# Kernel tuning notes

Measured on AMD Instinct MI355X. Metric: run time of the kernel, lower is better.

Reference implementation:

```python
import jax, jax.numpy as jnp
import numpy as np

B, S, D_MODEL, D_K, D_V = 4, 2048, 1024, 1024, 1024


def setup_inputs() -> dict:
    key = jax.random.key(0)
    k1, k2, k3, k4 = jax.random.split(key, 4)
    scale = 1.0 / np.sqrt(D_MODEL)
    x = jax.random.normal(k1, (B, S, D_MODEL), dtype=jnp.float32)
    Wq = jax.random.normal(k2, (D_K, D_MODEL), dtype=jnp.float32) * scale
    Wk = jax.random.normal(k3, (D_K, D_MODEL), dtype=jnp.float32) * scale
    Wv = jax.random.normal(k4, (D_V, D_MODEL), dtype=jnp.float32) * scale
    # causal mask: position i may attend to j <= i (True = keep)
    mask = jnp.broadcast_to(jnp.tril(jnp.ones((S, S), dtype=bool)), (B, S, S))
    return {"x": x, "mask": mask, "Wq": Wq, "Wk": Wk, "Wv": Wv}


def reference(x, mask, Wq, Wk, Wv):
    # nn.Linear(d, k, bias=False): y = x @ W.T with W of shape [k, d]
    q = jnp.einsum('bsd,kd->bsk', x, Wq)
    k = jnp.einsum('bsd,kd->bsk', x, Wk)
    v = jnp.einsum('bsd,vd->bsv', x, Wv)
    scores = jnp.einsum('bik,bjk->bij', q, k) / jnp.sqrt(jnp.float32(D_K))
    s = jnp.where(mask, scores, -jnp.inf)
    # masked, fully-masked-row-safe softmax (fully masked rows -> all zeros,
    # matching softmax[all-masked rows] = 0 in the original)
    m = jnp.max(s, axis=-1, keepdims=True)
    m_safe = jnp.where(jnp.isfinite(m), m, 0.0)
    e = jnp.exp(s - m_safe)          # exp(-inf) = 0 for masked entries
    denom = jnp.sum(e, axis=-1, keepdims=True)
    p = e / jnp.where(denom == 0.0, 1.0, denom)
    return jnp.einsum('bij,bjv->biv', p, v)
```

## Files before the change

### kernel.cpp

```cpp
#include <hip/hip_runtime.h>
#include <hip/hip_bf16.h>
#include <stdint.h>

#define SEQ   2048
#define DM    1024
#define NBAT  4

typedef __attribute__((ext_vector_type(8))) short  short8;
typedef __attribute__((ext_vector_type(4))) float  floatx4;

__device__ __forceinline__ unsigned short f2b(float f) {
    __hip_bfloat16 h = __float2bfloat16(f);
    unsigned short r;
    __builtin_memcpy(&r, &h, 2);
    return r;
}

__device__ __forceinline__ ushort4 pack4(float a, float b, float c, float d) {
    ushort4 u; u.x = f2b(a); u.y = f2b(b); u.z = f2b(c); u.w = f2b(d); return u;
}

__device__ __forceinline__ void gload16(const void* g, void* s) {
    __builtin_amdgcn_global_load_lds(
        (const __attribute__((address_space(1))) unsigned int*)(uintptr_t)g,
        (__attribute__((address_space(3))) unsigned int*)(uintptr_t)s,
        16, 0, 0);
}

__global__ void prep(const float4* __restrict__ x,
                     const float4* __restrict__ w0, const float4* __restrict__ w1,
                     const float4* __restrict__ w2,
                     ushort4* __restrict__ xb, ushort4* __restrict__ wall,
                     float* __restrict__ rsum)
{
    const int b = blockIdx.x;
    const int t = threadIdx.x;
    if (b < 8192) {
        const int i = b * 256 + t;
        float4 f = x[i];
        xb[i] = pack4(f.x, f.y, f.z, f.w);
    } else if (b < 11264) {
        const int idx  = b - 8192;
        const int wsel = idx >> 10;
        const int i    = (idx & 1023) * 256 + t;
        const float4* src = (wsel == 0) ? w0 : (wsel == 1) ? w1 : w2;
        float4 f = src[i];
        wall[(size_t)wsel * 262144 + i] = pack4(f.x, f.y, f.z, f.w);
    } else {
        rsum[(b - 11264) * 256 + t] = 0.f;
    }
}

#define SLOTS 24576

__global__ __launch_bounds__(512, 2) void qkv_gemm(
    const unsigned short* __restrict__ A, const unsigned short* __restrict__ Bm,
    unsigned short* __restrict__ Qo, unsigned short* __restrict__ Ko,
    unsigned short* __restrict__ Vto, float qscale)
{
    __shared__ __align__(16) unsigned short lds[3 * SLOTS];

    const int bid = blockIdx.x;
    const int wg  = (bid & 7) * 96 + (bid >> 3);
    const int mt  = wg / 24, nt = wg - mt * 24;
    const int m0  = mt * 256, n0 = nt * 128;

    const int t    = threadIdx.x;
    const int w    = t >> 6;
    const int lane = t & 63;
    const int wr   = w >> 1, wc = w & 1;
    const int r    = lane & 15, q = lane >> 4;

    const int srow = lane >> 3;
    const int scol = ((lane & 7) ^ srow) << 3;

    const int aoff = (wr >> 1) * 8192 + ((wr & 1) * 64 + r) * 64;
    const int boff = 16384 + (wc * 64 + r) * 64;
    const int sk0  = ((0 + q) ^ (r & 7)) * 8;
    const int sk1  = ((4 + q) ^ (r & 7)) * 8;

    floatx4 acc[4][4];
#pragma unroll
    for (int i = 0; i < 4; i++)
#pragma unroll
        for (int j = 0; j < 4; j++)
            acc[i][j] = (floatx4){0.f, 0.f, 0.f, 0.f};

#define STGA(KB, SL) do { \
    gload16(A + (((size_t)(m0 +       w * 16 + srow)) << 10) + (KB) + scol, &lds[(SL) +         w * 1024]); \
    gload16(A + (((size_t)(m0 +   8 + w * 16 + srow)) << 10) + (KB) + scol, &lds[(SL) +         w * 1024 + 512]); \
    gload16(A + (((size_t)(m0 + 128 + w * 16 + srow)) << 10) + (KB) + scol, &lds[(SL) + 8192 +  w * 1024]); \
    gload16(A + (((size_t)(m0 + 136 + w * 16 + srow)) << 10) + (KB) + scol, &lds[(SL) + 8192 +  w * 1024 + 512]); \
  } while (0)
#define STGB(KB, SL) do { \
    gload16(Bm + (((size_t)(n0 +      w * 16 + srow)) << 10) + (KB) + scol, &lds[(SL) + 16384 + w * 1024]); \
    gload16(Bm + (((size_t)(n0 +  8 + w * 16 + srow)) << 10) + (KB) + scol, &lds[(SL) + 16384 + w * 1024 + 512]); \
  } while (0)

    STGA(0, 0);
    STGB(0, 0);
    STGA(64, SLOTS);
    STGB(64, SLOTS);
    asm volatile("s_waitcnt vmcnt(6)" ::: "memory");
    __builtin_amdgcn_s_barrier();

    for (int tt = 0; tt < 16; ++tt) {
        const int sl  = (tt % 3) * SLOTS;
        const int nsl = ((tt + 2) % 3) * SLOTS;
        const int nkb = (tt + 2 < 16) ? (tt + 2) * 64 : 0;

        const int aB = sl + aoff;
        const int bB = sl + boff;
        short8 a00 = *(const short8*)&lds[aB + sk0 +    0];
        short8 a10 = *(const short8*)&lds[aB + sk0 + 1024];
        short8 a20 = *(const short8*)&lds[aB + sk0 + 2048];
        short8 a30 = *(const short8*)&lds[aB + sk0 + 3072];
        short8 b00 = *(const short8*)&lds[bB + sk0 +    0];
        short8 b10 = *(const short8*)&lds[bB + sk0 + 1024];
        short8 b20 = *(const short8*)&lds[bB + sk0 + 2048];
        short8 b30 = *(const short8*)&lds[bB + sk0 + 3072];
        short8 a01 = *(const short8*)&lds[aB + sk1 +    0];
        short8 a11 = *(const short8*)&lds[aB + sk1 + 1024];
        short8 a21 = *(const short8*)&lds[aB + sk1 + 2048];
        short8 a31 = *(const short8*)&lds[aB + sk1 + 3072];
        short8 b01 = *(const short8*)&lds[bB + sk1 +    0];
        short8 b11 = *(const short8*)&lds[bB + sk1 + 1024];
        short8 b21 = *(const short8*)&lds[bB + sk1 + 2048];
        short8 b31 = *(const short8*)&lds[bB + sk1 + 3072];

        STGA(nkb, nsl);
        STGB(nkb, nsl);
        asm volatile("s_waitcnt vmcnt(6)" ::: "memory");
        __builtin_amdgcn_s_barrier();

        __builtin_amdgcn_s_setprio(1);
        acc[0][0] = __builtin_amdgcn_mfma_f32_16x16x32_bf16(a00, b00, acc[0][0], 0, 0, 0);
        acc[0][1] = __builtin_amdgcn_mfma_f32_16x16x32_bf16(a00, b10, acc[0][1], 0, 0, 0);
        acc[0][2] = __builtin_amdgcn_mfma_f32_16x16x32_bf16(a00, b20, acc[0][2], 0, 0, 0);
        acc[0][3] = __builtin_amdgcn_mfma_f32_16x16x32_bf16(a00, b30, acc[0][3], 0, 0, 0);
        acc[1][0] = __builtin_amdgcn_mfma_f32_16x16x32_bf16(a10, b00, acc[1][0], 0, 0, 0);
        acc[1][1] = __builtin_amdgcn_mfma_f32_16x16x32_bf16(a10, b10, acc[1][1], 0, 0, 0);
        acc[1][2] = __builtin_amdgcn_mfma_f32_16x16x32_bf16(a10, b20, acc[1][2], 0, 0, 0);
        acc[1][3] = __builtin_amdgcn_mfma_f32_16x16x32_bf16(a10, b30, acc[1][3], 0, 0, 0);
        acc[2][0] = __builtin_amdgcn_mfma_f32_16x16x32_bf16(a20, b00, acc[2][0], 0, 0, 0);
        acc[2][1] = __builtin_amdgcn_mfma_f32_16x16x32_bf16(a20, b10, acc[2][1], 0, 0, 0);
        acc[2][2] = __builtin_amdgcn_mfma_f32_16x16x32_bf16(a20, b20, acc[2][2], 0, 0, 0);
        acc[2][3] = __builtin_amdgcn_mfma_f32_16x16x32_bf16(a20, b30, acc[2][3], 0, 0, 0);
        acc[3][0] = __builtin_amdgcn_mfma_f32_16x16x32_bf16(a30, b00, acc[3][0], 0, 0, 0);
        acc[3][1] = __builtin_amdgcn_mfma_f32_16x16x32_bf16(a30, b10, acc[3][1], 0, 0, 0);
        acc[3][2] = __builtin_amdgcn_mfma_f32_16x16x32_bf16(a30, b20, acc[3][2], 0, 0, 0);
        acc[3][3] = __builtin_amdgcn_mfma_f32_16x16x32_bf16(a30, b30, acc[3][3], 0, 0, 0);
        acc[0][0] = __builtin_amdgcn_mfma_f32_16x16x32_bf16(a01, b01, acc[0][0], 0, 0, 0);
        acc[0][1] = __builtin_amdgcn_mfma_f32_16x16x32_bf16(a01, b11, acc[0][1], 0, 0, 0);
        acc[0][2] = __builtin_amdgcn_mfma_f32_16x16x32_bf16(a01, b21, acc[0][2], 0, 0, 0);
        acc[0][3] = __builtin_amdgcn_mfma_f32_16x16x32_bf16(a01, b31, acc[0][3], 0, 0, 0);
        acc[1][0] = __builtin_amdgcn_mfma_f32_16x16x32_bf16(a11, b01, acc[1][0], 0, 0, 0);
        acc[1][1] = __builtin_amdgcn_mfma_f32_16x16x32_bf16(a11, b11, acc[1][1], 0, 0, 0);
        acc[1][2] = __builtin_amdgcn_mfma_f32_16x16x32_bf16(a11, b21, acc[1][2], 0, 0, 0);
        acc[1][3] = __builtin_amdgcn_mfma_f32_16x16x32_bf16(a11, b31, acc[1][3], 0, 0, 0);
        acc[2][0] = __builtin_amdgcn_mfma_f32_16x16x32_bf16(a21, b01, acc[2][0], 0, 0, 0);
        acc[2][1] = __builtin_amdgcn_mfma_f32_16x16x32_bf16(a21, b11, acc[2][1], 0, 0, 0);
        acc[2][2] = __builtin_amdgcn_mfma_f32_16x16x32_bf16(a21, b21, acc[2][2], 0, 0, 0);
        acc[2][3] = __builtin_amdgcn_mfma_f32_16x16x32_bf16(a21, b31, acc[2][3], 0, 0, 0);
        acc[3][0] = __builtin_amdgcn_mfma_f32_16x16x32_bf16(a31, b01, acc[3][0], 0, 0, 0);
        acc[3][1] = __builtin_amdgcn_mfma_f32_16x16x32_bf16(a31, b11, acc[3][1], 0, 0, 0);
        acc[3][2] = __builtin_amdgcn_mfma_f32_16x16x32_bf16(a31, b21, acc[3][2], 0, 0, 0);
        acc[3][3] = __builtin_amdgcn_mfma_f32_16x16x32_bf16(a31, b31, acc[3][3], 0, 0, 0);
        __builtin_amdgcn_s_setprio(0);
    }
#undef STGA
#undef STGB

    const int gmb = m0 + wr * 64 + q * 4;
    const int gnb = n0 + wc * 64 + r;
    if (nt < 8) {
#pragma unroll
        for (int i = 0; i < 4; i++) {
            const int gm = gmb + i * 16;
#pragma unroll
            for (int j = 0; j < 4; j++) {
                const int gn = gnb + j * 16;
#pragma unroll
                for (int rr = 0; rr < 4; rr++)
                    Qo[(size_t)(gm + rr) * 1024 + gn] = f2b(acc[i][j][rr] * qscale);
            }
        }
    } else if (nt < 16) {
#pragma unroll
        for (int i = 0; i < 4; i++) {
            const int gm = gmb + i * 16;
#pragma unroll
            for (int j = 0; j < 4; j++) {
                const int gn = gnb + j * 16;
#pragma unroll
                for (int rr = 0; rr < 4; rr++)
                    Ko[(size_t)(gm + rr) * 1024 + (gn - 1024)] = f2b(acc[i][j][rr]);
            }
        }
    } else {
#pragma unroll
        for (int i = 0; i < 4; i++) {
            const int gm = gmb + i * 16;
            const int b  = gm >> 11;
            const int s  = gm & 2047;
#pragma unroll
            for (int j = 0; j < 4; j++) {
                const int v = gnb + j * 16 - 2048;
                *(ushort4*)&Vto[((size_t)(b * 1024 + v)) * 2048 + s] =
                    pack4(acc[i][j][0], acc[i][j][1], acc[i][j][2], acc[i][j][3]);
            }
        }
    }
}

template<int MODE>
__global__ __launch_bounds__(512, 2) void attn256(
    const unsigned short* __restrict__ Ag, const unsigned short* __restrict__ Bg,
    void* __restrict__ Cv, float* __restrict__ rowsum)
{
    __shared__ __align__(16) unsigned short lds[3 * SLOTS];

    const int z = blockIdx.z;
    int m0, n0;
    if (MODE == 0) {
        const int f = blockIdx.x;
        int ti = (int)((sqrtf(4.f * f + 1.f) - 1.f) * 0.5f);
        while ((ti + 1) * (ti + 2) <= f) ti++;
        while (ti * (ti + 1) > f) ti--;
        const int tj = f - ti * (ti + 1);
        m0 = ti * 256;
        n0 = tj * 128;
    } else {
        m0 = (int)(gridDim.y - 1 - blockIdx.y) * 256;
        n0 = blockIdx.x * 128;
    }

    const size_t LDA = (MODE == 0) ? DM : SEQ;
    const size_t LDB = (MODE == 0) ? DM : SEQ;
    const unsigned short* A  = Ag + (size_t)z * ((MODE == 0) ? SEQ * DM : SEQ * SEQ);
    const unsigned short* Bm = Bg + (size_t)z * ((MODE == 0) ? SEQ * DM : DM * SEQ);
    const int NT = ((MODE == 0) ? DM : (m0 + 256)) / 64;

    const int t    = threadIdx.x;
    const int w    = t >> 6;
    const int lane = t & 63;
    const int wr   = w >> 1, wc = w & 1;
    const int r    = lane & 15, q = lane >> 4;

    const int srow = lane >> 3;
    const int scol = ((lane & 7) ^ srow) << 3;

    const int aoff = (wr >> 1) * 8192 + ((wr & 1) * 64 + r) * 64;
    const int boff = 16384 + (wc * 64 + r) * 64;
    const int sk0  = ((0 + q) ^ (r & 7)) * 8;
    const int sk1  = ((4 + q) ^ (r & 7)) * 8;

    floatx4 acc[4][4];
#pragma unroll
    for (int i = 0; i < 4; i++)
#pragma unroll
        for (int j = 0; j < 4; j++)
            acc[i][j] = (floatx4){0.f, 0.f, 0.f, 0.f};

#define ASTG(KB, SL) do { \
    gload16(A + (size_t)(m0 +       w * 16 + srow) * LDA + (KB) + scol, &lds[(SL) +         w * 1024]); \
    gload16(A + (size_t)(m0 +   8 + w * 16 + srow) * LDA + (KB) + scol, &lds[(SL) +         w * 1024 + 512]); \
    gload16(A + (size_t)(m0 + 128 + w * 16 + srow) * LDA + (KB) + scol, &lds[(SL) + 8192 +  w * 1024]); \
    gload16(A + (size_t)(m0 + 136 + w * 16 + srow) * LDA + (KB) + scol, &lds[(SL) + 8192 +  w * 1024 + 512]); \
  } while (0)
#define BSTG(KB, SL) do { \
    gload16(Bm + (size_t)(n0 +      w * 16 + srow) * LDB + (KB) + scol, &lds[(SL) + 16384 + w * 1024]); \
    gload16(Bm + (size_t)(n0 +  8 + w * 16 + srow) * LDB + (KB) + scol, &lds[(SL) + 16384 + w * 1024 + 512]); \
  } while (0)

    ASTG(0, 0);
    BSTG(0, 0);
    ASTG(64, SLOTS);
    BSTG(64, SLOTS);
    asm volatile("s_waitcnt vmcnt(6)" ::: "memory");
    __builtin_amdgcn_s_barrier();

    for (int tt = 0; tt < NT; ++tt) {
        const int sl  = (tt % 3) * SLOTS;
        const int nsl = ((tt + 2) % 3) * SLOTS;
        const int nkb = (tt + 2 < NT) ? (tt + 2) * 64 : 0;

        const int aB = sl + aoff;
        const int bB = sl + boff;
        short8 a00 = *(const short8*)&lds[aB + sk0 +    0];
        short8 a10 = *(const short8*)&lds[aB + sk0 + 1024];
        short8 a20 = *(const short8*)&lds[aB + sk0 + 2048];
        short8 a30 = *(const short8*)&lds[aB + sk0 + 3072];
        short8 b00 = *(const short8*)&lds[bB + sk0 +    0];
        short8 b10 = *(const short8*)&lds[bB + sk0 + 1024];
        short8 b20 = *(const short8*)&lds[bB + sk0 + 2048];
        short8 b30 = *(const short8*)&lds[bB + sk0 + 3072];
        short8 a01 = *(const short8*)&lds[aB + sk1 +    0];
        short8 a11 = *(const short8*)&lds[aB + sk1 + 1024];
        short8 a21 = *(const short8*)&lds[aB + sk1 + 2048];
        short8 a31 = *(const short8*)&lds[aB + sk1 + 3072];
        short8 b01 = *(const short8*)&lds[bB + sk1 +    0];
        short8 b11 = *(const short8*)&lds[bB + sk1 + 1024];
        short8 b21 = *(const short8*)&lds[bB + sk1 + 2048];
        short8 b31 = *(const short8*)&lds[bB + sk1 + 3072];

        ASTG(nkb, nsl);
        BSTG(nkb, nsl);
        asm volatile("s_waitcnt vmcnt(6)" ::: "memory");
        __builtin_amdgcn_s_barrier();

        __builtin_amdgcn_s_setprio(1);
        acc[0][0] = __builtin_amdgcn_mfma_f32_16x16x32_bf16(b00, a00, acc[0][0], 0, 0, 0);
        acc[0][1] = __builtin_amdgcn_mfma_f32_16x16x32_bf16(b10, a00, acc[0][1], 0, 0, 0);
        acc[0][2] = __builtin_amdgcn_mfma_f32_16x16x32_bf16(b20, a00, acc[0][2], 0, 0, 0);
        acc[0][3] = __builtin_amdgcn_mfma_f32_16x16x32_bf16(b30, a00, acc[0][3], 0, 0, 0);
        acc[1][0] = __builtin_amdgcn_mfma_f32_16x16x32_bf16(b00, a10, acc[1][0], 0, 0, 0);
        acc[1][1] = __builtin_amdgcn_mfma_f32_16x16x32_bf16(b10, a10, acc[1][1], 0, 0, 0);
        acc[1][2] = __builtin_amdgcn_mfma_f32_16x16x32_bf16(b20, a10, acc[1][2], 0, 0, 0);
        acc[1][3] = __builtin_amdgcn_mfma_f32_16x16x32_bf16(b30, a10, acc[1][3], 0, 0, 0);
        acc[2][0] = __builtin_amdgcn_mfma_f32_16x16x32_bf16(b00, a20, acc[2][0], 0, 0, 0);
        acc[2][1] = __builtin_amdgcn_mfma_f32_16x16x32_bf16(b10, a20, acc[2][1], 0, 0, 0);
        acc[2][2] = __builtin_amdgcn_mfma_f32_16x16x32_bf16(b20, a20, acc[2][2], 0, 0, 0);
        acc[2][3] = __builtin_amdgcn_mfma_f32_16x16x32_bf16(b30, a20, acc[2][3], 0, 0, 0);
        acc[3][0] = __builtin_amdgcn_mfma_f32_16x16x32_bf16(b00, a30, acc[3][0], 0, 0, 0);
        acc[3][1] = __builtin_amdgcn_mfma_f32_16x16x32_bf16(b10, a30, acc[3][1], 0, 0, 0);
        acc[3][2] = __builtin_amdgcn_mfma_f32_16x16x32_bf16(b20, a30, acc[3][2], 0, 0, 0);
        acc[3][3] = __builtin_amdgcn_mfma_f32_16x16x32_bf16(b30, a30, acc[3][3], 0, 0, 0);
        acc[0][0] = __builtin_amdgcn_mfma_f32_16x16x32_bf16(b01, a01, acc[0][0], 0, 0, 0);
        acc[0][1] = __builtin_amdgcn_mfma_f32_16x16x32_bf16(b11, a01, acc[0][1], 0, 0, 0);
        acc[0][2] = __builtin_amdgcn_mfma_f32_16x16x32_bf16(b21, a01, acc[0][2], 0, 0, 0);
        acc[0][3] = __builtin_amdgcn_mfma_f32_16x16x32_bf16(b31, a01, acc[0][3], 0, 0, 0);
        acc[1][0] = __builtin_amdgcn_mfma_f32_16x16x32_bf16(b01, a11, acc[1][0], 0, 0, 0);
        acc[1][1] = __builtin_amdgcn_mfma_f32_16x16x32_bf16(b11, a11, acc[1][1], 0, 0, 0);
        acc[1][2] = __builtin_amdgcn_mfma_f32_16x16x32_bf16(b21, a11, acc[1][2], 0, 0, 0);
        acc[1][3] = __builtin_amdgcn_mfma_f32_16x16x32_bf16(b31, a11, acc[1][3], 0, 0, 0);
        acc[2][0] = __builtin_amdgcn_mfma_f32_16x16x32_bf16(b01, a21, acc[2][0], 0, 0, 0);
        acc[2][1] = __builtin_amdgcn_mfma_f32_16x16x32_bf16(b11, a21, acc[2][1], 0, 0, 0);
        acc[2][2] = __builtin_amdgcn_mfma_f32_16x16x32_bf16(b21, a21, acc[2][2], 0, 0, 0);
        acc[2][3] = __builtin_amdgcn_mfma_f32_16x16x32_bf16(b31, a21, acc[2][3], 0, 0, 0);
        acc[3][0] = __builtin_amdgcn_mfma_f32_16x16x32_bf16(b01, a31, acc[3][0], 0, 0, 0);
        acc[3][1] = __builtin_amdgcn_mfma_f32_16x16x32_bf16(b11, a31, acc[3][1], 0, 0, 0);
        acc[3][2] = __builtin_amdgcn_mfma_f32_16x16x32_bf16(b21, a31, acc[3][2], 0, 0, 0);
        acc[3][3] = __builtin_amdgcn_mfma_f32_16x16x32_bf16(b31, a31, acc[3][3], 0, 0, 0);
        __builtin_amdgcn_s_setprio(0);
    }
#undef ASTG
#undef BSTG

    const int gmb = m0 + wr * 64 + r;
    const int gnb = n0 + wc * 64 + q * 4;
    if (MODE == 0) {
        unsigned short* E = (unsigned short*)Cv + (size_t)z * SEQ * SEQ;
        float* rs = rowsum + (size_t)z * SEQ;
#pragma unroll
        for (int i = 0; i < 4; i++) {
            const int gm = gmb + i * 16;
            float part = 0.f;
#pragma unroll
            for (int j = 0; j < 4; j++) {
                const int gn = gnb + j * 16;
                float e0 = (gn + 0 <= gm) ? __expf(acc[i][j][0]) : 0.f;
                float e1 = (gn + 1 <= gm) ? __expf(acc[i][j][1]) : 0.f;
                float e2 = (gn + 2 <= gm) ? __expf(acc[i][j][2]) : 0.f;
                float e3 = (gn + 3 <= gm) ? __expf(acc[i][j][3]) : 0.f;
                part += (e0 + e1) + (e2 + e3);
                *(ushort4*)&E[(size_t)gm * SEQ + gn] = pack4(e0, e1, e2, e3);
            }
            part += __shfl_xor(part, 16, 64);
            part += __shfl_xor(part, 32, 64);
            if (q == 0) atomicAdd(&rs[gm], part);
        }
    } else {
        float* C = (float*)Cv + (size_t)z * SEQ * DM;
        const float* rs = rowsum + (size_t)z * SEQ;
#pragma unroll
        for (int i = 0; i < 4; i++) {
            const int gm = gmb + i * 16;
            const float inv = 1.0f / rs[gm];
#pragma unroll
            for (int j = 0; j < 4; j++) {
                const int gn = gnb + j * 16;
                float4 o;
                o.x = acc[i][j][0] * inv;
                o.y = acc[i][j][1] * inv;
                o.z = acc[i][j][2] * inv;
                o.w = acc[i][j][3] * inv;
                *(float4*)&C[(size_t)gm * DM + gn] = o;
            }
        }
    }
}

extern "C" void kernel_launch(void* const* d_in, const int* in_sizes, int n_in,
                              void* d_out, int out_size, void* d_ws, size_t ws_size,
                              hipStream_t stream) {
    (void)in_sizes; (void)n_in; (void)out_size; (void)ws_size;
    const float* x  = (const float*)d_in[0];
    const float* Wq = (const float*)d_in[2];
    const float* Wk = (const float*)d_in[3];
    const float* Wv = (const float*)d_in[4];

    char* base = (char*)d_ws;
    size_t off = 0;
    auto alloc = [&](size_t n) { char* p = base + off; off += (n + 255) & ~(size_t)255; return p; };

    unsigned short* xb   = (unsigned short*)alloc((size_t)NBAT * SEQ * DM * 2);
    unsigned short* wall = (unsigned short*)alloc((size_t)3 * DM * DM * 2);
    unsigned short* Qb   = (unsigned short*)alloc((size_t)NBAT * SEQ * DM * 2);
    unsigned short* Kb   = (unsigned short*)alloc((size_t)NBAT * SEQ * DM * 2);
    unsigned short* Vtb  = (unsigned short*)alloc((size_t)NBAT * DM * SEQ * 2);
    unsigned short* E    = (unsigned short*)alloc((size_t)NBAT * SEQ * SEQ * 2);
    float*          rsum = (float*)alloc((size_t)NBAT * SEQ * 4);

    prep<<<dim3(11296), dim3(256), 0, stream>>>(
        (const float4*)x, (const float4*)Wq, (const float4*)Wk, (const float4*)Wv,
        (ushort4*)xb, (ushort4*)wall, rsum);

    qkv_gemm<<<dim3(768), dim3(512), 0, stream>>>(
        xb, wall, Qb, Kb, Vtb, 0.03125f);

    attn256<0><<<dim3(72, 1, NBAT), dim3(512), 0, stream>>>(Qb, Kb, E, rsum);

    attn256<1><<<dim3(DM / 128, SEQ / 256, NBAT), dim3(512), 0, stream>>>(E, Vtb, d_out, rsum);
}
```

Measured before the change: 260.5 us.

## Use 256x256 tiles with double buffering for QKV and QK^T GEMMs

Adds a new gemm256 kernel with 256x256 output tiles (8 waves, each holding an 8x4 MFMA accumulator grid) and a two-stage LDS double buffer. It replaces the 256x128 triple-buffered QKV projection and QK^T score kernels, halving their block counts. The larger tile raises arithmetic intensity and data reuse per load, at the cost of more accumulator registers and LDS per block. The causal QK^T kernel now runs on a triangular grid of 256x256 tiles. The PV kernel is kept with its original tiling.

```diff
diff --git a/kernel.cpp b/kernel.cpp
--- a/kernel.cpp
+++ b/kernel.cpp
@@ -51,19 +51,202 @@
     }
 }
 
+template<int EPI>
+__global__ __launch_bounds__(512, 2) void gemm256(
+    const unsigned short* __restrict__ Ag, const unsigned short* __restrict__ Bg,
+    void* __restrict__ P0, void* __restrict__ P1, void* __restrict__ P2,
+    float* __restrict__ rowsum, float qscale)
+{
+    __shared__ __align__(16) unsigned short lds[65536];
+
+    int m0, n0, ntl = 0, z = 0;
+    const unsigned short* A;
+    const unsigned short* Bm;
+
+    if (EPI == 0) {
+        const int bid = blockIdx.x;
+        const int wg  = (bid & 7) * 48 + (bid >> 3);
+        const int mt  = wg / 12; ntl = wg - mt * 12;
+        m0 = mt * 256; n0 = ntl * 256;
+        A = Ag; Bm = Bg;
+    } else {
+        z = blockIdx.z;
+        const int f = blockIdx.x;
+        int ti = (int)((sqrtf(8.f * f + 1.f) - 1.f) * 0.5f);
+        while ((ti + 1) * (ti + 2) / 2 <= f) ti++;
+        while (ti * (ti + 1) / 2 > f) ti--;
+        const int tj = f - ti * (ti + 1) / 2;
+        m0 = ti * 256; n0 = tj * 256;
+        A = Ag + (size_t)z * SEQ * DM; Bm = Bg + (size_t)z * SEQ * DM;
+    }
+
+    const int t    = threadIdx.x;
+    const int w    = t >> 6;
+    const int lane = t & 63;
+    const int wr   = w >> 2, wc = w & 3;
+    const int r    = lane & 15, q = lane >> 4;
+
+    const int srow = lane >> 3;
+    const int scol = ((lane & 7) ^ srow) << 3;
+
+    const int sk0 = ((0 + q) ^ (r & 7)) * 8;
+    const int sk1 = ((4 + q) ^ (r & 7)) * 8;
+    const int aRd = wr * 8192 + r * 64;
+    const int bRd = 16384 + (wc >> 1) * 8192 + ((wc & 1) * 64 + r) * 64;
+
+    floatx4 acc[8][4];
+#pragma unroll
+    for (int i = 0; i < 8; i++)
+#pragma unroll
+        for (int j = 0; j < 4; j++)
+            acc[i][j] = (floatx4){0.f, 0.f, 0.f, 0.f};
+
+#define STGC(G, R0, KB, CB) do { \
+    gload16((G) + (size_t)((R0) + w * 16 + srow)     * DM + (KB) + scol, &lds[(CB) + w * 1024]); \
+    gload16((G) + (size_t)((R0) + w * 16 + srow + 8) * DM + (KB) + scol, &lds[(CB) + w * 1024 + 512]); \
+  } while (0)
+#define STG4(KB, OB) do { \
+    STGC(A,  m0,       (KB), (OB)); \
+    STGC(A,  m0 + 128, (KB), (OB) + 8192); \
+    STGC(Bm, n0,       (KB), (OB) + 16384); \
+    STGC(Bm, n0 + 128, (KB), (OB) + 24576); \
+  } while (0)
+
+#define ONE_MFMA(AC, AF, BF) do { \
+    if (EPI == 0) (AC) = __builtin_amdgcn_mfma_f32_16x16x32_bf16((AF), (BF), (AC), 0, 0, 0); \
+    else          (AC) = __builtin_amdgcn_mfma_f32_16x16x32_bf16((BF), (AF), (AC), 0, 0, 0); \
+  } while (0)
+
+    STG4(0, 0);
+
+    for (int tt = 0; tt < 16; ++tt) {
+        const int cb  = (tt & 1) * 32768;
+        const int ob  = 32768 - cb;
+        const int nkb = (tt + 1 < 16 ? tt + 1 : 0) * 64;
+
+        asm volatile("s_waitcnt vmcnt(0)" ::: "memory");
+        __builtin_amdgcn_s_barrier();
+
+        short8 a0[8], b0[4];
+#pragma unroll
+        for (int i = 0; i < 8; i++)
+            a0[i] = *(const short8*)&lds[cb + aRd + i * 1024 + sk0];
+#pragma unroll
+        for (int j = 0; j < 4; j++)
+            b0[j] = *(const short8*)&lds[cb + bRd + j * 1024 + sk0];
+
+        STG4(nkb, ob);
+
+        __builtin_amdgcn_s_setprio(1);
+#pragma unroll
+        for (int i = 0; i < 8; i++)
+#pragma unroll
+            for (int j = 0; j < 4; j++)
+                ONE_MFMA(acc[i][j], a0[i], b0[j]);
+
+        short8 a1[8], b1[4];
+#pragma unroll
+        for (int i = 0; i < 8; i++)
+            a1[i] = *(const short8*)&lds[cb + aRd + i * 1024 + sk1];
+#pragma unroll
+        for (int j = 0; j < 4; j++)
+            b1[j] = *(const short8*)&lds[cb + bRd + j * 1024 + sk1];
+#pragma unroll
+        for (int i = 0; i < 8; i++)
+#pragma unroll
+            for (int j = 0; j < 4; j++)
+                ONE_MFMA(acc[i][j], a1[i], b1[j]);
+        __builtin_amdgcn_s_setprio(0);
+    }
+#undef STGC
+#undef STG4
+#undef ONE_MFMA
+
+    if (EPI == 0) {
+        const int gmb = m0 + wr * 128 + q * 4;
+        const int gnb = n0 + wc * 64 + r;
+        unsigned short* Qo  = (unsigned short*)P0;
+        unsigned short* Ko  = (unsigned short*)P1;
+        unsigned short* Vto = (unsigned short*)P2;
+        if (ntl < 4) {
+#pragma unroll
+            for (int i = 0; i < 8; i++) {
+                const int gm = gmb + i * 16;
+#pragma unroll
+                for (int j = 0; j < 4; j++) {
+                    const int gn = gnb + j * 16;
+#pragma unroll
+                    for (int rr = 0; rr < 4; rr++)
+                        Qo[(size_t)(gm + rr) * 1024 + gn] = f2b(acc[i][j][rr] * qscale);
+                }
+            }
+        } else if (ntl < 8) {
+#pragma unroll
+            for (int i = 0; i < 8; i++) {
+                const int gm = gmb + i * 16;
+#pragma unroll
+                for (int j = 0; j < 4; j++) {
+                    const int gn = gnb + j * 16;
+#pragma unroll
+                    for (int rr = 0; rr < 4; rr++)
+                        Ko[(size_t)(gm + rr) * 1024 + (gn - 1024)] = f2b(acc[i][j][rr]);
+                }
+            }
+        } else {
+#pragma unroll
+            for (int i = 0; i < 8; i++) {
+                const int gm = gmb + i * 16;
+                const int b  = gm >> 11;
+                const int s  = gm & 2047;
+#pragma unroll
+                for (int j = 0; j < 4; j++) {
+                    const int v = gnb + j * 16 - 2048;
+                    *(ushort4*)&Vto[((size_t)(b * 1024 + v)) * 2048 + s] =
+                        pack4(acc[i][j][0], acc[i][j][1], acc[i][j][2], acc[i][j][3]);
+                }
+            }
+        }
+    } else {
+        const int gmb = m0 + wr * 128 + r;
+        const int gnb = n0 + wc * 64 + q * 4;
+        unsigned short* E = (unsigned short*)P0 + (size_t)z * SEQ * SEQ;
+        float* rs = rowsum + (size_t)z * SEQ;
+#pragma unroll
+        for (int i = 0; i < 8; i++) {
+            const int gm = gmb + i * 16;
+            float part = 0.f;
+#pragma unroll
+            for (int j = 0; j < 4; j++) {
+                const int gn = gnb + j * 16;
+                float e0 = (gn + 0 <= gm) ? __expf(acc[i][j][0]) : 0.f;
+                float e1 = (gn + 1 <= gm) ? __expf(acc[i][j][1]) : 0.f;
+                float e2 = (gn + 2 <= gm) ? __expf(acc[i][j][2]) : 0.f;
+                float e3 = (gn + 3 <= gm) ? __expf(acc[i][j][3]) : 0.f;
+                part += (e0 + e1) + (e2 + e3);
+                *(ushort4*)&E[(size_t)gm * SEQ + gn] = pack4(e0, e1, e2, e3);
+            }
+            part += __shfl_xor(part, 16, 64);
+            part += __shfl_xor(part, 32, 64);
+            if (q == 0) atomicAdd(&rs[gm], part);
+        }
+    }
+}
+
 #define SLOTS 24576
 
-__global__ __launch_bounds__(512, 2) void qkv_gemm(
-    const unsigned short* __restrict__ A, const unsigned short* __restrict__ Bm,
-    unsigned short* __restrict__ Qo, unsigned short* __restrict__ Ko,
-    unsigned short* __restrict__ Vto, float qscale)
+__global__ __launch_bounds__(512, 2) void attn_pv(
+    const unsigned short* __restrict__ Ag, const unsigned short* __restrict__ Bg,
+    float* __restrict__ Cv, const float* __restrict__ rowsum)
 {
     __shared__ __align__(16) unsigned short lds[3 * SLOTS];
 
-    const int bid = blockIdx.x;
-    const int wg  = (bid & 7) * 96 + (bid >> 3);
-    const int mt  = wg / 24, nt = wg - mt * 24;
-    const int m0  = mt * 256, n0 = nt * 128;
+    const int z = blockIdx.z;
+    const int m0 = (int)(gridDim.y - 1 - blockIdx.y) * 256;
+    const int n0 = blockIdx.x * 128;
+
+    const unsigned short* A  = Ag + (size_t)z * SEQ * SEQ;
+    const unsigned short* Bm = Bg + (size_t)z * DM * SEQ;
+    const int NT = (m0 + 256) / 64;
 
     const int t    = threadIdx.x;
     const int w    = t >> 6;
@@ -86,191 +269,15 @@
         for (int j = 0; j < 4; j++)
             acc[i][j] = (floatx4){0.f, 0.f, 0.f, 0.f};
 
-#define STGA(KB, SL) do { \
-    gload16(A + (((size_t)(m0 +       w * 16 + srow)) << 10) + (KB) + scol, &lds[(SL) +         w * 1024]); \
-    gload16(A + (((size_t)(m0 +   8 + w * 16 + srow)) << 10) + (KB) + scol, &lds[(SL) +         w * 1024 + 512]); \
-    gload16(A + (((size_t)(m0 + 128 + w * 16 + srow)) << 10) + (KB) + scol, &lds[(SL) + 8192 +  w * 1024]); \
-    gload16(A + (((size_t)(m0 + 136 + w * 16 + srow)) << 10) + (KB) + scol, &lds[(SL) + 8192 +  w * 1024 + 512]); \
-  } while (0)
-#define STGB(KB, SL) do { \
-    gload16(Bm + (((size_t)(n0 +      w * 16 + srow)) << 10) + (KB) + scol, &lds[(SL) + 16384 + w * 1024]); \
-    gload16(Bm + (((size_t)(n0 +  8 + w * 16 + srow)) << 10) + (KB) + scol, &lds[(SL) + 16384 + w * 1024 + 512]); \
-  } while (0)
-
-    STGA(0, 0);
-    STGB(0, 0);
-    STGA(64, SLOTS);
-    STGB(64, SLOTS);
-    asm volatile("s_waitcnt vmcnt(6)" ::: "memory");
-    __builtin_amdgcn_s_barrier();
-
-    for (int tt = 0; tt < 16; ++tt) {
-        const int sl  = (tt % 3) * SLOTS;
-        const int nsl = ((tt + 2) % 3) * SLOTS;
-        const int nkb = (tt + 2 < 16) ? (tt + 2) * 64 : 0;
-
-        const int aB = sl + aoff;
-        const int bB = sl + boff;
-        short8 a00 = *(const short8*)&lds[aB + sk0 +    0];
-        short8 a10 = *(const short8*)&lds[aB + sk0 + 1024];
-        short8 a20 = *(const short8*)&lds[aB + sk0 + 2048];
-        short8 a30 = *(const short8*)&lds[aB + sk0 + 3072];
-        short8 b00 = *(const short8*)&lds[bB + sk0 +    0];
-        short8 b10 = *(const short8*)&lds[bB + sk0 + 1024];
-        short8 b20 = *(const short8*)&lds[bB + sk0 + 2048];
-        short8 b30 = *(const short8*)&lds[bB + sk0 + 3072];
-        short8 a01 = *(const short8*)&lds[aB + sk1 +    0];
-        short8 a11 = *(const short8*)&lds[aB + sk1 + 1024];
-        short8 a21 = *(const short8*)&lds[aB + sk1 + 2048];
-        short8 a31 = *(const short8*)&lds[aB + sk1 + 3072];
-        short8 b01 = *(const short8*)&lds[bB + sk1 +    0];
-        short8 b11 = *(const short8*)&lds[bB + sk1 + 1024];
-        short8 b21 = *(const short8*)&lds[bB + sk1 + 2048];
-        short8 b31 = *(const short8*)&lds[bB + sk1 + 3072];
-
-        STGA(nkb, nsl);
-        STGB(nkb, nsl);
-        asm volatile("s_waitcnt vmcnt(6)" ::: "memory");
-        __builtin_amdgcn_s_barrier();
-
-        __builtin_amdgcn_s_setprio(1);
-        acc[0][0] = __builtin_amdgcn_mfma_f32_16x16x32_bf16(a00, b00, acc[0][0], 0, 0, 0);
-        acc[0][1] = __builtin_amdgcn_mfma_f32_16x16x32_bf16(a00, b10, acc[0][1], 0, 0, 0);
-        acc[0][2] = __builtin_amdgcn_mfma_f32_16x16x32_bf16(a00, b20, acc[0][2], 0, 0, 0);
-        acc[0][3] = __builtin_amdgcn_mfma_f32_16x16x32_bf16(a00, b30, acc[0][3], 0, 0, 0);
-        acc[1][0] = __builtin_amdgcn_mfma_f32_16x16x32_bf16(a10, b00, acc[1][0], 0, 0, 0);
-        acc[1][1] = __builtin_amdgcn_mfma_f32_16x16x32_bf16(a10, b10, acc[1][1], 0, 0, 0);
-        acc[1][2] = __builtin_amdgcn_mfma_f32_16x16x32_bf16(a10, b20, acc[1][2], 0, 0, 0);
-        acc[1][3] = __builtin_amdgcn_mfma_f32_16x16x32_bf16(a10, b30, acc[1][3], 0, 0, 0);
-        acc[2][0] = __builtin_amdgcn_mfma_f32_16x16x32_bf16(a20, b00, acc[2][0], 0, 0, 0);
-        acc[2][1] = __builtin_amdgcn_mfma_f32_16x16x32_bf16(a20, b10, acc[2][1], 0, 0, 0);
-        acc[2][2] = __builtin_amdgcn_mfma_f32_16x16x32_bf16(a20, b20, acc[2][2], 0, 0, 0);
-        acc[2][3] = __builtin_amdgcn_mfma_f32_16x16x32_bf16(a20, b30, acc[2][3], 0, 0, 0);
-        acc[3][0] = __builtin_amdgcn_mfma_f32_16x16x32_bf16(a30, b00, acc[3][0], 0, 0, 0);
-        acc[3][1] = __builtin_amdgcn_mfma_f32_16x16x32_bf16(a30, b10, acc[3][1], 0, 0, 0);
-        acc[3][2] = __builtin_amdgcn_mfma_f32_16x16x32_bf16(a30, b20, acc[3][2], 0, 0, 0);
-        acc[3][3] = __builtin_amdgcn_mfma_f32_16x16x32_bf16(a30, b30, acc[3][3], 0, 0, 0);
-        acc[0][0] = __builtin_amdgcn_mfma_f32_16x16x32_bf16(a01, b01, acc[0][0], 0, 0, 0);
-        acc[0][1] = __builtin_amdgcn_mfma_f32_16x16x32_bf16(a01, b11, acc[0][1], 0, 0, 0);
-        acc[0][2] = __builtin_amdgcn_mfma_f32_16x16x32_bf16(a01, b21, acc[0][2], 0, 0, 0);
-        acc[0][3] = __builtin_amdgcn_mfma_f32_16x16x32_bf16(a01, b31, acc[0][3], 0, 0, 0);
-        acc[1][0] = __builtin_amdgcn_mfma_f32_16x16x32_bf16(a11, b01, acc[1][0], 0, 0, 0);
-        acc[1][1] = __builtin_amdgcn_mfma_f32_16x16x32_bf16(a11, b11, acc[1][1], 0, 0, 0);
-        acc[1][2] = __builtin_amdgcn_mfma_f32_16x16x32_bf16(a11, b21, acc[1][2], 0, 0, 0);
-        acc[1][3] = __builtin_amdgcn_mfma_f32_16x16x32_bf16(a11, b31, acc[1][3], 0, 0, 0);
-        acc[2][0] = __builtin_amdgcn_mfma_f32_16x16x32_bf16(a21, b01, acc[2][0], 0, 0, 0);
-        acc[2][1] = __builtin_amdgcn_mfma_f32_16x16x32_bf16(a21, b11, acc[2][1], 0, 0, 0);
-        acc[2][2] = __builtin_amdgcn_mfma_f32_16x16x32_bf16(a21, b21, acc[2][2], 0, 0, 0);
-        acc[2][3] = __builtin_amdgcn_mfma_f32_16x16x32_bf16(a21, b31, acc[2][3], 0, 0, 0);
-        acc[3][0] = __builtin_amdgcn_mfma_f32_16x16x32_bf16(a31, b01, acc[3][0], 0, 0, 0);
-        acc[3][1] = __builtin_amdgcn_mfma_f32_16x16x32_bf16(a31, b11, acc[3][1], 0, 0, 0);
-        acc[3][2] = __builtin_amdgcn_mfma_f32_16x16x32_bf16(a31, b21, acc[3][2], 0, 0, 0);
-        acc[3][3] = __builtin_amdgcn_mfma_f32_16x16x32_bf16(a31, b31, acc[3][3], 0, 0, 0);
-        __builtin_amdgcn_s_setprio(0);
-    }
-#undef STGA
-#undef STGB
-
-    const int gmb = m0 + wr * 64 + q * 4;
-    const int gnb = n0 + wc * 64 + r;
-    if (nt < 8) {
-#pragma unroll
-        for (int i = 0; i < 4; i++) {
-            const int gm = gmb + i * 16;
-#pragma unroll
-            for (int j = 0; j < 4; j++) {
-                const int gn = gnb + j * 16;
-#pragma unroll
-                for (int rr = 0; rr < 4; rr++)
-                    Qo[(size_t)(gm + rr) * 1024 + gn] = f2b(acc[i][j][rr] * qscale);
-            }
-        }
-    } else if (nt < 16) {
-#pragma unroll
-        for (int i = 0; i < 4; i++) {
-            const int gm = gmb + i * 16;
-#pragma unroll
-            for (int j = 0; j < 4; j++) {
-                const int gn = gnb + j * 16;
-#pragma unroll
-                for (int rr = 0; rr < 4; rr++)
-                    Ko[(size_t)(gm + rr) * 1024 + (gn - 1024)] = f2b(acc[i][j][rr]);
-            }
-        }
-    } else {
-#pragma unroll
-        for (int i = 0; i < 4; i++) {
-            const int gm = gmb + i * 16;
-            const int b  = gm >> 11;
-            const int s  = gm & 2047;
-#pragma unroll
-            for (int j = 0; j < 4; j++) {
-                const int v = gnb + j * 16 - 2048;
-                *(ushort4*)&Vto[((size_t)(b * 1024 + v)) * 2048 + s] =
-                    pack4(acc[i][j][0], acc[i][j][1], acc[i][j][2], acc[i][j][3]);
-            }
-        }
-    }
-}
-
-template<int MODE>
-__global__ __launch_bounds__(512, 2) void attn256(
-    const unsigned short* __restrict__ Ag, const unsigned short* __restrict__ Bg,
-    void* __restrict__ Cv, float* __restrict__ rowsum)
-{
-    __shared__ __align__(16) unsigned short lds[3 * SLOTS];
-
-    const int z = blockIdx.z;
-    int m0, n0;
-    if (MODE == 0) {
-        const int f = blockIdx.x;
-        int ti = (int)((sqrtf(4.f * f + 1.f) - 1.f) * 0.5f);
-        while ((ti + 1) * (ti + 2) <= f) ti++;
-        while (ti * (ti + 1) > f) ti--;
-        const int tj = f - ti * (ti + 1);
-        m0 = ti * 256;
-        n0 = tj * 128;
-    } else {
-        m0 = (int)(gridDim.y - 1 - blockIdx.y) * 256;
-        n0 = blockIdx.x * 128;
-    }
-
-    const size_t LDA = (MODE == 0) ? DM : SEQ;
-    const size_t LDB = (MODE == 0) ? DM : SEQ;
-    const unsigned short* A  = Ag + (size_t)z * ((MODE == 0) ? SEQ * DM : SEQ * SEQ);
-    const unsigned short* Bm = Bg + (size_t)z * ((MODE == 0) ? SEQ * DM : DM * SEQ);
-    const int NT = ((MODE == 0) ? DM : (m0 + 256)) / 64;
-
-    const int t    = threadIdx.x;
-    const int w    = t >> 6;
-    const int lane = t & 63;
-    const int wr   = w >> 1, wc = w & 1;
-    const int r    = lane & 15, q = lane >> 4;
-
-    const int srow = lane >> 3;
-    const int scol = ((lane & 7) ^ srow) << 3;
-
-    const int aoff = (wr >> 1) * 8192 + ((wr & 1) * 64 + r) * 64;
-    const int boff = 16384 + (wc * 64 + r) * 64;
-    const int sk0  = ((0 + q) ^ (r & 7)) * 8;
-    const int sk1  = ((4 + q) ^ (r & 7)) * 8;
-
-    floatx4 acc[4][4];
-#pragma unroll
-    for (int i = 0; i < 4; i++)
-#pragma unroll
-        for (int j = 0; j < 4; j++)
-            acc[i][j] = (floatx4){0.f, 0.f, 0.f, 0.f};
-
 #define ASTG(KB, SL) do { \
-    gload16(A + (size_t)(m0 +       w * 16 + srow) * LDA + (KB) + scol, &lds[(SL) +         w * 1024]); \
-    gload16(A + (size_t)(m0 +   8 + w * 16 + srow) * LDA + (KB) + scol, &lds[(SL) +         w * 1024 + 512]); \
-    gload16(A + (size_t)(m0 + 128 + w * 16 + srow) * LDA + (KB) + scol, &lds[(SL) + 8192 +  w * 1024]); \
-    gload16(A + (size_t)(m0 + 136 + w * 16 + srow) * LDA + (KB) + scol, &lds[(SL) + 8192 +  w * 1024 + 512]); \
+    gload16(A + (size_t)(m0 +       w * 16 + srow) * SEQ + (KB) + scol, &lds[(SL) +         w * 1024]); \
+    gload16(A + (size_t)(m0 +   8 + w * 16 + srow) * SEQ + (KB) + scol, &lds[(SL) +         w * 1024 + 512]); \
+    gload16(A + (size_t)(m0 + 128 + w * 16 + srow) * SEQ + (KB) + scol, &lds[(SL) + 8192 +  w * 1024]); \
+    gload16(A + (size_t)(m0 + 136 + w * 16 + srow) * SEQ + (KB) + scol, &lds[(SL) + 8192 +  w * 1024 + 512]); \
   } while (0)
 #define BSTG(KB, SL) do { \
-    gload16(Bm + (size_t)(n0 +      w * 16 + srow) * LDB + (KB) + scol, &lds[(SL) + 16384 + w * 1024]); \
-    gload16(Bm + (size_t)(n0 +  8 + w * 16 + srow) * LDB + (KB) + scol, &lds[(SL) + 16384 + w * 1024 + 512]); \
+    gload16(Bm + (size_t)(n0 +      w * 16 + srow) * SEQ + (KB) + scol, &lds[(SL) + 16384 + w * 1024]); \
+    gload16(Bm + (size_t)(n0 +  8 + w * 16 + srow) * SEQ + (KB) + scol, &lds[(SL) + 16384 + w * 1024 + 512]); \
   } while (0)
 
     ASTG(0, 0);
@@ -349,44 +356,21 @@
 
     const int gmb = m0 + wr * 64 + r;
     const int gnb = n0 + wc * 64 + q * 4;
-    if (MODE == 0) {
-        unsigned short* E = (unsigned short*)Cv + (size_t)z * SEQ * SEQ;
-        float* rs = rowsum + (size_t)z * SEQ;
-#pragma unroll
-        for (int i = 0; i < 4; i++) {
-            const int gm = gmb + i * 16;
-            float part = 0.f;
-#pragma unroll
-            for (int j = 0; j < 4; j++) {
-                const int gn = gnb + j * 16;
-                float e0 = (gn + 0 <= gm) ? __expf(acc[i][j][0]) : 0.f;
-                float e1 = (gn + 1 <= gm) ? __expf(acc[i][j][1]) : 0.f;
-                float e2 = (gn + 2 <= gm) ? __expf(acc[i][j][2]) : 0.f;
-                float e3 = (gn + 3 <= gm) ? __expf(acc[i][j][3]) : 0.f;
-                part += (e0 + e1) + (e2 + e3);
-                *(ushort4*)&E[(size_t)gm * SEQ + gn] = pack4(e0, e1, e2, e3);
-            }
-            part += __shfl_xor(part, 16, 64);
-            part += __shfl_xor(part, 32, 64);
-            if (q == 0) atomicAdd(&rs[gm], part);
-        }
-    } else {
-        float* C = (float*)Cv + (size_t)z * SEQ * DM;
-        const float* rs = rowsum + (size_t)z * SEQ;
-#pragma unroll
-        for (int i = 0; i < 4; i++) {
-            const int gm = gmb + i * 16;
-            const float inv = 1.0f / rs[gm];
-#pragma unroll
-            for (int j = 0; j < 4; j++) {
-                const int gn = gnb + j * 16;
-                float4 o;
-                o.x = acc[i][j][0] * inv;
-                o.y = acc[i][j][1] * inv;
-                o.z = acc[i][j][2] * inv;
-                o.w = acc[i][j][3] * inv;
-                *(float4*)&C[(size_t)gm * DM + gn] = o;
-            }
+    float* C = Cv + (size_t)z * SEQ * DM;
+    const float* rs = rowsum + (size_t)z * SEQ;
+#pragma unroll
+    for (int i = 0; i < 4; i++) {
+        const int gm = gmb + i * 16;
+        const float inv = 1.0f / rs[gm];
+#pragma unroll
+        for (int j = 0; j < 4; j++) {
+            const int gn = gnb + j * 16;
+            float4 o;
+            o.x = acc[i][j][0] * inv;
+            o.y = acc[i][j][1] * inv;
+            o.z = acc[i][j][2] * inv;
+            o.w = acc[i][j][3] * inv;
+            *(float4*)&C[(size_t)gm * DM + gn] = o;
         }
     }
 }
@@ -416,10 +400,12 @@
         (const float4*)x, (const float4*)Wq, (const float4*)Wk, (const float4*)Wv,
         (ushort4*)xb, (ushort4*)wall, rsum);
 
-    qkv_gemm<<<dim3(768), dim3(512), 0, stream>>>(
-        xb, wall, Qb, Kb, Vtb, 0.03125f);
-
-    attn256<0><<<dim3(72, 1, NBAT), dim3(512), 0, stream>>>(Qb, Kb, E, rsum);
-
-    attn256<1><<<dim3(DM / 128, SEQ / 256, NBAT), dim3(512), 0, stream>>>(E, Vtb, d_out, rsum);
-}
+    gemm256<0><<<dim3(384), dim3(512), 0, stream>>>(
+        xb, wall, Qb, Kb, Vtb, nullptr, 0.03125f);
+
+    gemm256<1><<<dim3(36, 1, NBAT), dim3(512), 0, stream>>>(
+        Qb, Kb, E, nullptr, nullptr, rsum, 0.f);
+
+    attn_pv<<<dim3(DM / 128, SEQ / 256, NBAT), dim3(512), 0, stream>>>(
+        E, Vtb, (float*)d_out, rsum);
+}
```

Result: no change. 257.2 us (-1.2%).
